# Performance work log

Measured on AMD Instinct MI355X. Metric: run time of the kernel, lower is better.

The kernel has to match this reference:

```python
import jax, jax.numpy as jnp
import numpy as np

N = 100000
E = 1600000
IN_DIM = 128
H = 64
OUT_DIM = 64
EPS = 1e-5


def batch_norm(x, gamma, beta):
    # BatchNorm1d with batch statistics (training-mode normalization, biased var)
    mu = jnp.mean(x, axis=0)
    var = jnp.var(x, axis=0)
    return (x - mu) * jax.lax.rsqrt(var + EPS) * gamma + beta


def gcn_conv(x, src, dst, W, b, n_nodes):
    # PyG GCNConv: add self-loops, symmetric deg^-1/2 normalization, X W, scatter-add, bias
    loop = jnp.arange(n_nodes, dtype=src.dtype)
    s = jnp.concatenate([src, loop])
    d = jnp.concatenate([dst, loop])
    w = jnp.ones(s.shape[0], dtype=x.dtype)
    deg = jax.ops.segment_sum(w, d, num_segments=n_nodes)
    dinv = jnp.where(deg > 0, jax.lax.rsqrt(deg), 0.0)
    norm = dinv[s] * w * dinv[d]                      # [E+N]
    h = x @ W                                         # [N, out]
    msg = h[s] * norm[:, None]                        # [E+N, out]
    out = jax.ops.segment_sum(msg, d, num_segments=n_nodes)
    return out + b


def setup_inputs() -> dict:
    key = jax.random.key(0)
    ks = jax.random.split(key, 12)
    x = jax.random.normal(ks[0], (N, IN_DIM), dtype=jnp.float32)
    edge_index = jax.random.randint(ks[1], (2, E), 0, N, dtype=jnp.int64)
    s = 0.05
    return {
        "x": x,
        "edge_index": edge_index,
        "bn_in_g": jnp.ones((IN_DIM,), jnp.float32),
        "bn_in_b": jnp.zeros((IN_DIM,), jnp.float32),
        "Wp": jax.random.normal(ks[2], (IN_DIM, H), jnp.float32) * s,
        "bp": jnp.zeros((H,), jnp.float32),
        "W1": jax.random.normal(ks[3], (H, H), jnp.float32) * s,
        "b1": jnp.zeros((H,), jnp.float32),
        "bn1_g": jnp.ones((H,), jnp.float32),
        "bn1_b": jnp.zeros((H,), jnp.float32),
        "W2": jax.random.normal(ks[4], (H, OUT_DIM), jnp.float32) * s,
        "b2": jnp.zeros((OUT_DIM,), jnp.float32),
        "bn2_g": jnp.ones((OUT_DIM,), jnp.float32),
        "bn2_b": jnp.zeros((OUT_DIM,), jnp.float32),
    }


def reference(x, edge_index, bn_in_g, bn_in_b, Wp, bp, W1, b1, bn1_g, bn1_b, W2, b2, bn2_g, bn2_b):
    src, dst = edge_index[0], edge_index[1]
    n = x.shape[0]
    h0 = batch_norm(x, bn_in_g, bn_in_b)
    h0 = jax.nn.relu(h0 @ Wp + bp)
    h1 = gcn_conv(h0, src, dst, W1, b1, n)
    h1 = jax.nn.relu(batch_norm(h1, bn1_g, bn1_b))
    # dropout in eval mode: identity
    h2 = gcn_conv(h1, src, dst, W2, b2, n)
    return batch_norm(h2, bn2_g, bn2_b)
```

## Files before the change

kernel.cpp:

```cpp
#include <hip/hip_runtime.h>
#include <hip/hip_bf16.h>

#define EPS 1e-5f
#define CAP 6144
#define PCHUNK 4096
#define XP 68

__device__ __forceinline__ void acc_q(float* acc, uint2 v, float s) {
    acc[0] += s * (float)((int)(v.x << 24) >> 24);
    acc[1] += s * (float)((int)(v.x << 16) >> 24);
    acc[2] += s * (float)((int)(v.x << 8) >> 24);
    acc[3] += s * (float)((int)v.x >> 24);
    acc[4] += s * (float)((int)(v.y << 24) >> 24);
    acc[5] += s * (float)((int)(v.y << 16) >> 24);
    acc[6] += s * (float)((int)(v.y << 8) >> 24);
    acc[7] += s * (float)((int)v.y >> 24);
}

#define GEMM_KK(kk, wvec)                                                        \
    {                                                                            \
        float a0 = (kk == 0) ? xv0.x : (kk == 1) ? xv0.y : (kk == 2) ? xv0.z : xv0.w; \
        float a1 = (kk == 0) ? xv1.x : (kk == 1) ? xv1.y : (kk == 2) ? xv1.z : xv1.w; \
        float a2 = (kk == 0) ? xv2.x : (kk == 1) ? xv2.y : (kk == 2) ? xv2.z : xv2.w; \
        float a3 = (kk == 0) ? xv3.x : (kk == 1) ? xv3.y : (kk == 2) ? xv3.z : xv3.w; \
        acc[0][0] += a0 * wvec.x; acc[0][1] += a0 * wvec.y;                      \
        acc[0][2] += a0 * wvec.z; acc[0][3] += a0 * wvec.w;                      \
        acc[1][0] += a1 * wvec.x; acc[1][1] += a1 * wvec.y;                      \
        acc[1][2] += a1 * wvec.z; acc[1][3] += a1 * wvec.w;                      \
        acc[2][0] += a2 * wvec.x; acc[2][1] += a2 * wvec.y;                      \
        acc[2][2] += a2 * wvec.z; acc[2][3] += a2 * wvec.w;                      \
        acc[3][0] += a3 * wvec.x; acc[3][1] += a3 * wvec.y;                      \
        acc[3][2] += a3 * wvec.z; acc[3][3] += a3 * wvec.w;                      \
    }

__global__ void k_init(int* __restrict__ cur, float* __restrict__ stats) {
    int t = threadIdx.x;
    stats[t] = 0.0f;
    cur[t] = t * CAP;
}

__global__ __launch_bounds__(256) void k_A(
    const int* __restrict__ src, const int* __restrict__ dst,
    int* __restrict__ cur, unsigned* __restrict__ packbuf, int E, int NBP,
    const float* __restrict__ x, float* __restrict__ xsum, float* __restrict__ xsq, int N) {
    __shared__ int h[512], delta[512], wsc[4];
    __shared__ unsigned buf[PCHUNK];
    __shared__ int addr[PCHUNK];
    int tx = threadIdx.x;
    if ((int)blockIdx.x < NBP) {
        int e0 = blockIdx.x * PCHUNK;
        int e1 = min(e0 + PCHUNK, E);
        int csize = e1 - e0;
        h[tx] = 0; h[tx + 256] = 0;
        __syncthreads();
        for (int e = e0 + tx; e < e1; e += 256)
            atomicAdd(&h[dst[e] >> 8], 1);
        __syncthreads();
        int b0 = tx * 2;
        int c0 = h[b0], c1 = h[b0 + 1];
        int tsum = c0 + c1;
        int lane = tx & 63, wid = tx >> 6;
        int v = tsum;
#pragma unroll
        for (int off = 1; off < 64; off <<= 1) {
            int u = __shfl_up(v, off);
            if (lane >= off) v += u;
        }
        if (lane == 63) wsc[wid] = v;
        __syncthreads();
        int wbase = 0;
        for (int w = 0; w < wid; w++) wbase += wsc[w];
        int excl0 = wbase + v - tsum;
        int excl1 = excl0 + c0;
        if (c0 > 0) delta[b0] = atomicAdd(&cur[b0], c0) - excl0;
        if (c1 > 0) delta[b0 + 1] = atomicAdd(&cur[b0 + 1], c1) - excl1;
        __syncthreads();
        h[b0] = excl0; h[b0 + 1] = excl1;
        __syncthreads();
        for (int e = e0 + tx; e < e1; e += 256) {
            int d = dst[e];
            int b = d >> 8;
            int rank = atomicAdd(&h[b], 1);
            buf[rank] = ((unsigned)src[e] << 8) | (unsigned)(d & 255);
            addr[rank] = delta[b];
        }
        __syncthreads();
        for (int i = tx; i < csize; i += 256)
            packbuf[addr[i] + i] = buf[i];
    } else {
        float* ls = (float*)buf;
        float* lq = ls + 256;
        int b2 = blockIdx.x - NBP;
        int col = tx & 127, half = tx >> 7;
        float s = 0.f, q = 0.f;
        for (int r = b2 * 2 + half; r < N; r += 1024) {
            float v = x[(long long)r * 128 + col];
            s += v; q += v * v;
        }
        ls[tx] = s; lq[tx] = q;
        __syncthreads();
        if (half == 0) {
            s = ls[tx] + ls[tx + 128];
            q = lq[tx] + lq[tx + 128];
            atomicAdd(&xsum[col], s);
            atomicAdd(&xsq[col], q);
        }
    }
}

__global__ __launch_bounds__(512) void k_B(
    const unsigned* __restrict__ packbuf, const int* __restrict__ cur,
    int2* __restrict__ rowbe, int* __restrict__ rowmid, float* __restrict__ dinv,
    int* __restrict__ eidx, int NB, int N, int Nh,
    const float* __restrict__ x, const float* __restrict__ stats,
    const float* __restrict__ g, const float* __restrict__ bbn,
    const float* __restrict__ Wp, const float* __restrict__ bp,
    float* __restrict__ H, float invN) {
    __shared__ __align__(16) char smem[52224];
    int tx = threadIdx.x;
    if ((int)blockIdx.x < NB) {
        int* cnt  = (int*)smem;
        int* loff = cnt + 512;
        int* wsum = loff + 512;
        int b = blockIdx.x;
        int base = b * CAP;
        int end = cur[b];
        cnt[tx] = 0;
        __syncthreads();
        for (int e = base + tx; e < end; e += 512) {
            unsigned pk = packbuf[e];
            int key = (((int)pk & 255) << 1) | (int)((pk >> 8) >= (unsigned)Nh);
            atomicAdd(&cnt[key], 1);
        }
        __syncthreads();
        int c = cnt[tx];
        int lane = tx & 63, wid = tx >> 6;
        int v = c;
#pragma unroll
        for (int off = 1; off < 64; off <<= 1) {
            int u = __shfl_up(v, off);
            if (lane >= off) v += u;
        }
        if (lane == 63) wsum[wid] = v;
        __syncthreads();
        int wbase = 0;
        for (int w = 0; w < wid; w++) wbase += wsum[w];
        int excl = wbase + v - c;
        loff[tx] = excl;
        __syncthreads();
        if (tx < 256) {
            int node = b * 256 + tx;
            if (node < N) {
                int beg = base + loff[2 * tx];
                int mid = base + loff[2 * tx + 1];
                int e2 = mid + cnt[2 * tx + 1];
                rowbe[node] = make_int2(beg, e2);
                rowmid[node] = mid;
                int deg = cnt[2 * tx] + cnt[2 * tx + 1];
                dinv[node] = rsqrtf(1.0f + (float)deg);
            }
        }
        __syncthreads();
        for (int e = base + tx; e < end; e += 512) {
            unsigned pk = packbuf[e];
            int key = (((int)pk & 255) << 1) | (int)((pk >> 8) >= (unsigned)Nh);
            int pos = atomicAdd(&loff[key], 1);
            eidx[base + pos] = (int)(pk >> 8);
        }
    } else {
        float* xs  = (float*)smem;
        float* ws  = xs + 128 * XP;
        float* scb = ws + 4096;
        float* shb = scb + 128;
        if (tx < 128) {
            float mu = stats[tx] * invN;
            float var = stats[128 + tx] * invN - mu * mu;
            float s = g[tx] * rsqrtf(var + EPS);
            scb[tx] = s;
            shb[tx] = bbn[tx] - mu * s;
        }
        __syncthreads();
        int r0 = ((int)blockIdx.x - NB) * 128;
        int cw = tx & 15, rw = tx >> 4;
        float acc[4][4];
#pragma unroll
        for (int j = 0; j < 4; j++)
#pragma unroll
            for (int i = 0; i < 4; i++) acc[j][i] = 0.f;

#pragma unroll 1
        for (int kc = 0; kc < 128; kc += 64) {
#pragma unroll
            for (int i = 0; i < 4; i++) {
                int f = tx + 512 * i;
                int row = f >> 4, kq = f & 15;
                int rr = r0 + row;
                float4 v = make_float4(0.f, 0.f, 0.f, 0.f);
                if (rr < N) v = ((const float4*)(x + (long long)rr * 128 + kc))[kq];
                int cb = kc + kq * 4;
                v.x = v.x * scb[cb + 0] + shb[cb + 0];
                v.y = v.y * scb[cb + 1] + shb[cb + 1];
                v.z = v.z * scb[cb + 2] + shb[cb + 2];
                v.w = v.w * scb[cb + 3] + shb[cb + 3];
                *(float4*)&xs[row * XP + kq * 4] = v;
            }
#pragma unroll
            for (int i = 0; i < 2; i++) {
                int f = tx + 512 * i;
                int k = f >> 4, cq = f & 15;
                float4 w = ((const float4*)(Wp + (long long)(kc + k) * 64))[cq];
                *(float4*)&ws[k * 64 + cq * 4] = w;
            }
            __syncthreads();
#pragma unroll 1
            for (int k4 = 0; k4 < 16; k4++) {
                float4 xv0 = *(const float4*)&xs[(rw * 4 + 0) * XP + k4 * 4];
                float4 xv1 = *(const float4*)&xs[(rw * 4 + 1) * XP + k4 * 4];
                float4 xv2 = *(const float4*)&xs[(rw * 4 + 2) * XP + k4 * 4];
                float4 xv3 = *(const float4*)&xs[(rw * 4 + 3) * XP + k4 * 4];
#pragma unroll
                for (int kk = 0; kk < 4; kk++) {
                    float4 w = *(const float4*)&ws[(k4 * 4 + kk) * 64 + cw * 4];
                    GEMM_KK(kk, w);
                }
            }
            __syncthreads();
        }
        float4 bpv = ((const float4*)bp)[cw];
#pragma unroll
        for (int j = 0; j < 4; j++) {
            int rr = r0 + rw * 4 + j;
            if (rr < N) {
                float4 o;
                o.x = fmaxf(acc[j][0] + bpv.x, 0.f);
                o.y = fmaxf(acc[j][1] + bpv.y, 0.f);
                o.z = fmaxf(acc[j][2] + bpv.z, 0.f);
                o.w = fmaxf(acc[j][3] + bpv.w, 0.f);
                ((float4*)(H + (long long)rr * 64))[cw] = o;
            }
        }
    }
}

template <bool BNRELU>
__global__ __launch_bounds__(512) void k_gemm_scale(
    const float* __restrict__ In, const float* __restrict__ W,
    const float* __restrict__ dinv, const float* __restrict__ ssum,
    const float* __restrict__ ssq, const float* __restrict__ g,
    const float* __restrict__ bb, float invN, unsigned* __restrict__ Bq,
    float* __restrict__ S, int N) {
    __shared__ __align__(16) char smem[52224];
    float* xs  = (float*)smem;
    float* ws  = xs + 128 * XP;
    float* scb = ws + 4096;
    float* shb = scb + 128;
    int tx = threadIdx.x;
    if (BNRELU) {
        if (tx < 64) {
            float mu = ssum[tx] * invN;
            float var = ssq[tx] * invN - mu * mu;
            float s = g[tx] * rsqrtf(var + EPS);
            scb[tx] = s;
            shb[tx] = bb[tx] - mu * s;
        }
        __syncthreads();
    }
    int r0 = blockIdx.x * 128;
    int cw = tx & 15, rw = tx >> 4;
#pragma unroll
    for (int i = 0; i < 4; i++) {
        int f = tx + 512 * i;
        int row = f >> 4, kq = f & 15;
        int rr = r0 + row;
        float4 v = make_float4(0.f, 0.f, 0.f, 0.f);
        if (rr < N) v = ((const float4*)(In + (long long)rr * 64))[kq];
        if (BNRELU) {
            int cb = kq * 4;
            v.x = fmaxf(v.x * scb[cb + 0] + shb[cb + 0], 0.f);
            v.y = fmaxf(v.y * scb[cb + 1] + shb[cb + 1], 0.f);
            v.z = fmaxf(v.z * scb[cb + 2] + shb[cb + 2], 0.f);
            v.w = fmaxf(v.w * scb[cb + 3] + shb[cb + 3], 0.f);
        }
        *(float4*)&xs[row * XP + kq * 4] = v;
    }
#pragma unroll
    for (int i = 0; i < 2; i++) {
        int f = tx + 512 * i;
        int k = f >> 4, cq = f & 15;
        float4 w = ((const float4*)(W + (long long)k * 64))[cq];
        *(float4*)&ws[k * 64 + cq * 4] = w;
    }
    __syncthreads();
    float acc[4][4];
#pragma unroll
    for (int j = 0; j < 4; j++)
#pragma unroll
        for (int i = 0; i < 4; i++) acc[j][i] = 0.f;
#pragma unroll 1
    for (int k4 = 0; k4 < 16; k4++) {
        float4 xv0 = *(const float4*)&xs[(rw * 4 + 0) * XP + k4 * 4];
        float4 xv1 = *(const float4*)&xs[(rw * 4 + 1) * XP + k4 * 4];
        float4 xv2 = *(const float4*)&xs[(rw * 4 + 2) * XP + k4 * 4];
        float4 xv3 = *(const float4*)&xs[(rw * 4 + 3) * XP + k4 * 4];
#pragma unroll
        for (int kk = 0; kk < 4; kk++) {
            float4 w = *(const float4*)&ws[(k4 * 4 + kk) * 64 + cw * 4];
            GEMM_KK(kk, w);
        }
    }
#pragma unroll
    for (int j = 0; j < 4; j++) {
        int rr = r0 + rw * 4 + j;
        float dv = (rr < N) ? dinv[rr] : 0.f;
        float m = 0.f;
#pragma unroll
        for (int i = 0; i < 4; i++) {
            acc[j][i] *= dv;
            m = fmaxf(m, fabsf(acc[j][i]));
        }
#pragma unroll
        for (int mask = 1; mask < 16; mask <<= 1)
            m = fmaxf(m, __shfl_xor(m, mask, 64));
        float inv = (m > 0.f) ? (127.0f / m) : 0.f;
        if (rr < N) {
            if (cw == 0) S[rr] = m * (1.0f / 127.0f);
            int q0 = (int)rintf(acc[j][0] * inv);
            int q1 = (int)rintf(acc[j][1] * inv);
            int q2 = (int)rintf(acc[j][2] * inv);
            int q3 = (int)rintf(acc[j][3] * inv);
            unsigned w = ((unsigned)q0 & 255u) | (((unsigned)q1 & 255u) << 8) |
                         (((unsigned)q2 & 255u) << 16) | (((unsigned)q3 & 255u) << 24);
            Bq[(long long)rr * 16 + cw] = w;
        }
    }
}

__global__ __launch_bounds__(256) void k_gather_finish(
    const uint2* __restrict__ Q, const float* __restrict__ S,
    const int2* __restrict__ rowbe, const int* __restrict__ rowmid,
    const int* __restrict__ eidx,
    const float* __restrict__ dinv, const float* __restrict__ bias,
    float* __restrict__ Out, float* __restrict__ ssum, float* __restrict__ ssq,
    int N, int Nh) {
    int tx = threadIdx.x;
    int g = tx >> 3;
    int l = tx & 7;
    int d = blockIdx.x * 32 + g;

    float s[8], q[8];
#pragma unroll
    for (int j = 0; j < 8; j++) { s[j] = 0.f; q[j] = 0.f; }

    if (d < N) {
        int2 be = rowbe[d];
        int mid = rowmid[d];
        uint2 v0 = Q[(long long)d * 8 + l];
        float sd = S[d];
        float dv = dinv[d];

        float acc[8];
#pragma unroll
        for (int j = 0; j < 8; j++) acc[j] = 0.f;

        for (int seg = 0; seg < 2; seg++) {
            int k  = seg ? mid : be.x;
            int ke = seg ? be.y : mid;
            if (k >= ke) continue;
            int dmy = seg ? Nh : 0;
            int idx_cur[8];
#pragma unroll
            for (int j = 0; j < 8; j++)
                idx_cur[j] = (k + j < ke) ? eidx[k + j] : dmy;

            while (k < ke) {
                uint2 bb[8];
                float sv[8];
#pragma unroll
                for (int j = 0; j < 8; j++)
                    bb[j] = Q[(long long)idx_cur[j] * 8 + l];
#pragma unroll
                for (int j = 0; j < 8; j++)
                    sv[j] = (k + j < ke) ? S[idx_cur[j]] : 0.f;
                int kn = k + 8;
                int idx_nxt[8];
#pragma unroll
                for (int j = 0; j < 8; j++)
                    idx_nxt[j] = (kn + j < ke) ? eidx[kn + j] : dmy;
#pragma unroll
                for (int j = 0; j < 8; j++)
                    acc_q(acc, bb[j], sv[j]);
#pragma unroll
                for (int j = 0; j < 8; j++) idx_cur[j] = idx_nxt[j];
                k = kn;
            }
        }
        acc_q(acc, v0, sd);

        float4 o0, o1;
#pragma unroll
        for (int j = 0; j < 8; j++) {
            float v = acc[j] * dv + bias[8 * l + j];
            ((j < 4) ? (&o0.x)[j] : (&o1.x)[j - 4]) = v;
            s[j] += v; q[j] += v * v;
        }
        float4* outp = (float4*)(Out + (long long)d * 64 + 8 * l);
        outp[0] = o0;
        outp[1] = o1;
    }

#pragma unroll
    for (int m = 8; m <= 32; m <<= 1) {
#pragma unroll
        for (int j = 0; j < 8; j++) {
            s[j] += __shfl_xor(s[j], m, 64);
            q[j] += __shfl_xor(q[j], m, 64);
        }
    }
    __shared__ float ws_s[4][64], ws_q[4][64];
    int wv = tx >> 6, ln = tx & 63;
    if (ln < 8) {
#pragma unroll
        for (int j = 0; j < 8; j++) {
            ws_s[wv][ln * 8 + j] = s[j];
            ws_q[wv][ln * 8 + j] = q[j];
        }
    }
    __syncthreads();
    if (tx < 64) {
        float S2 = ws_s[0][tx] + ws_s[1][tx] + ws_s[2][tx] + ws_s[3][tx];
        float Q2 = ws_q[0][tx] + ws_q[1][tx] + ws_q[2][tx] + ws_q[3][tx];
        atomicAdd(&ssum[tx], S2);
        atomicAdd(&ssq[tx], Q2);
    }
}

__global__ __launch_bounds__(256) void k_final(const float* __restrict__ In,
                                               const float* __restrict__ ssum,
                                               const float* __restrict__ ssq,
                                               const float* __restrict__ g,
                                               const float* __restrict__ bb, float invN,
                                               float* __restrict__ out, int total4) {
    __shared__ float scs[64], shs[64];
    int tx = threadIdx.x;
    if (tx < 64) {
        float mu = ssum[tx] * invN;
        float var = ssq[tx] * invN - mu * mu;
        float s = g[tx] * rsqrtf(var + EPS);
        scs[tx] = s;
        shs[tx] = bb[tx] - mu * s;
    }
    __syncthreads();
    int t = blockIdx.x * blockDim.x + tx;
    if (t < total4) {
        float4 v = ((const float4*)In)[t];
        int j = (t * 4) & 63;
        v.x = v.x * scs[j + 0] + shs[j + 0];
        v.y = v.y * scs[j + 1] + shs[j + 1];
        v.z = v.z * scs[j + 2] + shs[j + 2];
        v.w = v.w * scs[j + 3] + shs[j + 3];
        ((float4*)out)[t] = v;
    }
}

extern "C" void kernel_launch(void* const* d_in, const int* in_sizes, int n_in,
                              void* d_out, int out_size, void* d_ws, size_t ws_size,
                              hipStream_t stream) {
    const float* x       = (const float*)d_in[0];
    const int*   ei      = (const int*)d_in[1];
    const float* bn_in_g = (const float*)d_in[2];
    const float* bn_in_b = (const float*)d_in[3];
    const float* Wp      = (const float*)d_in[4];
    const float* bp      = (const float*)d_in[5];
    const float* W1      = (const float*)d_in[6];
    const float* b1      = (const float*)d_in[7];
    const float* bn1_g   = (const float*)d_in[8];
    const float* bn1_b   = (const float*)d_in[9];
    const float* W2      = (const float*)d_in[10];
    const float* b2      = (const float*)d_in[11];
    const float* bn2_g   = (const float*)d_in[12];
    const float* bn2_b   = (const float*)d_in[13];

    int N = in_sizes[0] / 128;
    int E = in_sizes[1] / 2;
    const int* src = ei;
    const int* dst = ei + E;
    int Nh  = N >> 1;
    int NB  = (N + 255) >> 8;
    int NBP = (E + PCHUNK - 1) / PCHUNK;
    int ntg = (N + 127) / 128;

    long long Npad = ((long long)N + 128) & ~127LL;
    int*   cur    = (int*)d_ws;
    float* stats  = (float*)(cur + 512);
    int2*  rowbe  = (int2*)(stats + 512);
    float* dinv   = (float*)(rowbe + Npad);
    int*   rowmid = (int*)(dinv + Npad);
    float* S      = (float*)(rowmid + Npad);
    unsigned* packbuf = (unsigned*)(S + Npad);
    int*   eidx   = (int*)(packbuf + (long long)NB * CAP);
    unsigned* Bq  = (unsigned*)(eidx + (long long)NB * CAP);
    float* H      = (float*)d_out;

    int gb = (N + 31) / 32;
    float invN = 1.0f / (float)N;

    k_init<<<1, 512, 0, stream>>>(cur, stats);
    k_A<<<NBP + 512, 256, 0, stream>>>(src, dst, cur, packbuf, E, NBP,
                                       x, stats, stats + 128, N);
    k_B<<<NB + ntg, 512, 0, stream>>>(packbuf, cur, rowbe, rowmid, dinv, eidx, NB, N, Nh,
                                      x, stats, bn_in_g, bn_in_b, Wp, bp, H, invN);

    k_gemm_scale<false><<<ntg, 512, 0, stream>>>(H, W1, dinv, nullptr, nullptr, nullptr,
                                                 nullptr, invN, Bq, S, N);
    k_gather_finish<<<gb, 256, 0, stream>>>((const uint2*)Bq, S, rowbe, rowmid, eidx, dinv,
                                            b1, H, stats + 256, stats + 320, N, Nh);

    k_gemm_scale<true><<<ntg, 512, 0, stream>>>(H, W2, dinv, stats + 256, stats + 320,
                                                bn1_g, bn1_b, invN, Bq, S, N);
    k_gather_finish<<<gb, 256, 0, stream>>>((const uint2*)Bq, S, rowbe, rowmid, eidx, dinv,
                                            b2, H, stats + 384, stats + 448, N, Nh);

    k_final<<<(N * 16 + 255) / 256, 256, 0, stream>>>(H, stats + 384, stats + 448,
                                                      bn2_g, bn2_b, invN, H, N * 16);
}
```

Measured before the change: 432.5 us.

## Split GCN gather into two passes over source-index halves for cache locality

The single gather kernel, which walked both edge segments (sources below and above Nh) per destination row, is split into two launches. The first pass gathers only the low-half sources and writes partial sums to H. The second pass reloads those partials, gathers the high-half sources, then applies dinv, bias and the batch-norm statistics. The aim is to keep each pass's gather working set (half of the quantized feature table) resident in cache, at the cost of an extra launch and an extra read and write of H.

```diff
diff --git a/kernel.cpp b/kernel.cpp
--- a/kernel.cpp
+++ b/kernel.cpp
@@ -335,12 +335,13 @@
     }
 }
 
-__global__ __launch_bounds__(256) void k_gather_finish(
+template <int PASS>
+__global__ __launch_bounds__(256) void k_gather_pass(
     const uint2* __restrict__ Q, const float* __restrict__ S,
     const int2* __restrict__ rowbe, const int* __restrict__ rowmid,
     const int* __restrict__ eidx,
     const float* __restrict__ dinv, const float* __restrict__ bias,
-    float* __restrict__ Out, float* __restrict__ ssum, float* __restrict__ ssq,
+    float* __restrict__ H, float* __restrict__ ssum, float* __restrict__ ssq,
     int N, int Nh) {
     int tx = threadIdx.x;
     int g = tx >> 3;
@@ -348,30 +349,37 @@
     int d = blockIdx.x * 32 + g;
 
     float s[8], q[8];
-#pragma unroll
-    for (int j = 0; j < 8; j++) { s[j] = 0.f; q[j] = 0.f; }
+    if (PASS == 1) {
+#pragma unroll
+        for (int j = 0; j < 8; j++) { s[j] = 0.f; q[j] = 0.f; }
+    }
 
     if (d < N) {
         int2 be = rowbe[d];
         int mid = rowmid[d];
-        uint2 v0 = Q[(long long)d * 8 + l];
-        float sd = S[d];
-        float dv = dinv[d];
-
         float acc[8];
-#pragma unroll
-        for (int j = 0; j < 8; j++) acc[j] = 0.f;
-
-        for (int seg = 0; seg < 2; seg++) {
-            int k  = seg ? mid : be.x;
-            int ke = seg ? be.y : mid;
-            if (k >= ke) continue;
-            int dmy = seg ? Nh : 0;
+        float4* hp = (float4*)(H + (long long)d * 64 + 8 * l);
+
+        int k, ke, dmy;
+        if (PASS == 0) {
+            uint2 v0 = Q[(long long)d * 8 + l];
+            float sd = S[d];
+#pragma unroll
+            for (int j = 0; j < 8; j++) acc[j] = 0.f;
+            acc_q(acc, v0, sd);
+            k = be.x; ke = mid; dmy = 0;
+        } else {
+            float4 p0 = hp[0], p1 = hp[1];
+            acc[0] = p0.x; acc[1] = p0.y; acc[2] = p0.z; acc[3] = p0.w;
+            acc[4] = p1.x; acc[5] = p1.y; acc[6] = p1.z; acc[7] = p1.w;
+            k = mid; ke = be.y; dmy = Nh;
+        }
+
+        if (k < ke) {
             int idx_cur[8];
 #pragma unroll
             for (int j = 0; j < 8; j++)
                 idx_cur[j] = (k + j < ke) ? eidx[k + j] : dmy;
-
             while (k < ke) {
                 uint2 bb[8];
                 float sv[8];
@@ -394,43 +402,52 @@
                 k = kn;
             }
         }
-        acc_q(acc, v0, sd);
-
-        float4 o0, o1;
-#pragma unroll
-        for (int j = 0; j < 8; j++) {
-            float v = acc[j] * dv + bias[8 * l + j];
-            ((j < 4) ? (&o0.x)[j] : (&o1.x)[j - 4]) = v;
-            s[j] += v; q[j] += v * v;
-        }
-        float4* outp = (float4*)(Out + (long long)d * 64 + 8 * l);
-        outp[0] = o0;
-        outp[1] = o1;
-    }
-
-#pragma unroll
-    for (int m = 8; m <= 32; m <<= 1) {
-#pragma unroll
-        for (int j = 0; j < 8; j++) {
-            s[j] += __shfl_xor(s[j], m, 64);
-            q[j] += __shfl_xor(q[j], m, 64);
-        }
-    }
-    __shared__ float ws_s[4][64], ws_q[4][64];
-    int wv = tx >> 6, ln = tx & 63;
-    if (ln < 8) {
-#pragma unroll
-        for (int j = 0; j < 8; j++) {
-            ws_s[wv][ln * 8 + j] = s[j];
-            ws_q[wv][ln * 8 + j] = q[j];
-        }
-    }
-    __syncthreads();
-    if (tx < 64) {
-        float S2 = ws_s[0][tx] + ws_s[1][tx] + ws_s[2][tx] + ws_s[3][tx];
-        float Q2 = ws_q[0][tx] + ws_q[1][tx] + ws_q[2][tx] + ws_q[3][tx];
-        atomicAdd(&ssum[tx], S2);
-        atomicAdd(&ssq[tx], Q2);
+
+        if (PASS == 0) {
+            float4 o0, o1;
+            o0.x = acc[0]; o0.y = acc[1]; o0.z = acc[2]; o0.w = acc[3];
+            o1.x = acc[4]; o1.y = acc[5]; o1.z = acc[6]; o1.w = acc[7];
+            hp[0] = o0;
+            hp[1] = o1;
+        } else {
+            float dv = dinv[d];
+            float4 o0, o1;
+#pragma unroll
+            for (int j = 0; j < 8; j++) {
+                float v = acc[j] * dv + bias[8 * l + j];
+                ((j < 4) ? (&o0.x)[j] : (&o1.x)[j - 4]) = v;
+                s[j] += v; q[j] += v * v;
+            }
+            hp[0] = o0;
+            hp[1] = o1;
+        }
+    }
+
+    if (PASS == 1) {
+#pragma unroll
+        for (int m = 8; m <= 32; m <<= 1) {
+#pragma unroll
+            for (int j = 0; j < 8; j++) {
+                s[j] += __shfl_xor(s[j], m, 64);
+                q[j] += __shfl_xor(q[j], m, 64);
+            }
+        }
+        __shared__ float ws_s[4][64], ws_q[4][64];
+        int wv = tx >> 6, ln = tx & 63;
+        if (ln < 8) {
+#pragma unroll
+            for (int j = 0; j < 8; j++) {
+                ws_s[wv][ln * 8 + j] = s[j];
+                ws_q[wv][ln * 8 + j] = q[j];
+            }
+        }
+        __syncthreads();
+        if (tx < 64) {
+            float S2 = ws_s[0][tx] + ws_s[1][tx] + ws_s[2][tx] + ws_s[3][tx];
+            float Q2 = ws_q[0][tx] + ws_q[1][tx] + ws_q[2][tx] + ws_q[3][tx];
+            atomicAdd(&ssum[tx], S2);
+            atomicAdd(&ssq[tx], Q2);
+        }
     }
 }
 
@@ -512,13 +529,17 @@
 
     k_gemm_scale<false><<<ntg, 512, 0, stream>>>(H, W1, dinv, nullptr, nullptr, nullptr,
                                                  nullptr, invN, Bq, S, N);
-    k_gather_finish<<<gb, 256, 0, stream>>>((const uint2*)Bq, S, rowbe, rowmid, eidx, dinv,
-                                            b1, H, stats + 256, stats + 320, N, Nh);
+    k_gather_pass<0><<<gb, 256, 0, stream>>>((const uint2*)Bq, S, rowbe, rowmid, eidx,
+                                             dinv, b1, H, stats + 256, stats + 320, N, Nh);
+    k_gather_pass<1><<<gb, 256, 0, stream>>>((const uint2*)Bq, S, rowbe, rowmid, eidx,
+                                             dinv, b1, H, stats + 256, stats + 320, N, Nh);
 
     k_gemm_scale<true><<<ntg, 512, 0, stream>>>(H, W2, dinv, stats + 256, stats + 320,
                                                 bn1_g, bn1_b, invN, Bq, S, N);
-    k_gather_finish<<<gb, 256, 0, stream>>>((const uint2*)Bq, S, rowbe, rowmid, eidx, dinv,
-                                            b2, H, stats + 384, stats + 448, N, Nh);
+    k_gather_pass<0><<<gb, 256, 0, stream>>>((const uint2*)Bq, S, rowbe, rowmid, eidx,
+                                             dinv, b2, H, stats + 384, stats + 448, N, Nh);
+    k_gather_pass<1><<<gb, 256, 0, stream>>>((const uint2*)Bq, S, rowbe, rowmid, eidx,
+                                             dinv, b2, H, stats + 384, stats + 448, N, Nh);
 
     k_final<<<(N * 16 + 255) / 256, 256, 0, stream>>>(H, stats + 384, stats + 448,
                                                       bn2_g, bn2_b, invN, H, N * 16);
```

Measured after the change: 468.6 us. 1.08x slower.

## Fuse first GCN weight GEMM and int8 quantization into projection kernel

Applied to the files above, without the earlier changes.

The projection GEMM blocks in k_B now keep the ReLU output tile in shared memory, multiply it by W1 directly, and write per-row int8-quantized rows plus row scales. This removes the separate k_gemm_scale pass and the round trip of the 100k x 64 float intermediate through global memory. The dinv scaling, which in k_B is not yet available to GEMM blocks because it is computed concurrently by the CSR blocks, moves to a new small k_scale kernel. The cost is more shared-memory work and longer GEMM blocks inside the mixed k_B launch.

```diff
diff --git a/kernel.cpp b/kernel.cpp
--- a/kernel.cpp
+++ b/kernel.cpp
@@ -115,7 +115,8 @@
     const float* __restrict__ x, const float* __restrict__ stats,
     const float* __restrict__ g, const float* __restrict__ bbn,
     const float* __restrict__ Wp, const float* __restrict__ bp,
-    float* __restrict__ H, float invN) {
+    const float* __restrict__ W1, unsigned* __restrict__ Bq, float* __restrict__ S,
+    float invN) {
     __shared__ __align__(16) char smem[52224];
     int tx = threadIdx.x;
     if ((int)blockIdx.x < NB) {
@@ -229,17 +230,65 @@
         float4 bpv = ((const float4*)bp)[cw];
 #pragma unroll
         for (int j = 0; j < 4; j++) {
+            float4 o;
+            o.x = fmaxf(acc[j][0] + bpv.x, 0.f);
+            o.y = fmaxf(acc[j][1] + bpv.y, 0.f);
+            o.z = fmaxf(acc[j][2] + bpv.z, 0.f);
+            o.w = fmaxf(acc[j][3] + bpv.w, 0.f);
+            *(float4*)&xs[(rw * 4 + j) * XP + cw * 4] = o;
+        }
+#pragma unroll
+        for (int i = 0; i < 2; i++) {
+            int f = tx + 512 * i;
+            int k = f >> 4, cq = f & 15;
+            float4 w = ((const float4*)(W1 + (long long)k * 64))[cq];
+            *(float4*)&ws[k * 64 + cq * 4] = w;
+        }
+        __syncthreads();
+#pragma unroll
+        for (int j = 0; j < 4; j++)
+#pragma unroll
+            for (int i = 0; i < 4; i++) acc[j][i] = 0.f;
+#pragma unroll 1
+        for (int k4 = 0; k4 < 16; k4++) {
+            float4 xv0 = *(const float4*)&xs[(rw * 4 + 0) * XP + k4 * 4];
+            float4 xv1 = *(const float4*)&xs[(rw * 4 + 1) * XP + k4 * 4];
+            float4 xv2 = *(const float4*)&xs[(rw * 4 + 2) * XP + k4 * 4];
+            float4 xv3 = *(const float4*)&xs[(rw * 4 + 3) * XP + k4 * 4];
+#pragma unroll
+            for (int kk = 0; kk < 4; kk++) {
+                float4 w = *(const float4*)&ws[(k4 * 4 + kk) * 64 + cw * 4];
+                GEMM_KK(kk, w);
+            }
+        }
+#pragma unroll
+        for (int j = 0; j < 4; j++) {
             int rr = r0 + rw * 4 + j;
+            float m = 0.f;
+#pragma unroll
+            for (int i = 0; i < 4; i++) m = fmaxf(m, fabsf(acc[j][i]));
+#pragma unroll
+            for (int mask = 1; mask < 16; mask <<= 1)
+                m = fmaxf(m, __shfl_xor(m, mask, 64));
+            float inv = (m > 0.f) ? (127.0f / m) : 0.f;
             if (rr < N) {
-                float4 o;
-                o.x = fmaxf(acc[j][0] + bpv.x, 0.f);
-                o.y = fmaxf(acc[j][1] + bpv.y, 0.f);
-                o.z = fmaxf(acc[j][2] + bpv.z, 0.f);
-                o.w = fmaxf(acc[j][3] + bpv.w, 0.f);
-                ((float4*)(H + (long long)rr * 64))[cw] = o;
-            }
-        }
-    }
+                if (cw == 0) S[rr] = m * (1.0f / 127.0f);
+                int q0 = (int)rintf(acc[j][0] * inv);
+                int q1 = (int)rintf(acc[j][1] * inv);
+                int q2 = (int)rintf(acc[j][2] * inv);
+                int q3 = (int)rintf(acc[j][3] * inv);
+                unsigned w = ((unsigned)q0 & 255u) | (((unsigned)q1 & 255u) << 8) |
+                             (((unsigned)q2 & 255u) << 16) | (((unsigned)q3 & 255u) << 24);
+                Bq[(long long)rr * 16 + cw] = w;
+            }
+        }
+    }
+}
+
+__global__ __launch_bounds__(256) void k_scale(float* __restrict__ S,
+                                               const float* __restrict__ dinv, int N) {
+    int r = blockIdx.x * 256 + threadIdx.x;
+    if (r < N) S[r] *= dinv[r];
 }
 
 template <bool BNRELU>
@@ -508,10 +557,8 @@
     k_A<<<NBP + 512, 256, 0, stream>>>(src, dst, cur, packbuf, E, NBP,
                                        x, stats, stats + 128, N);
     k_B<<<NB + ntg, 512, 0, stream>>>(packbuf, cur, rowbe, rowmid, dinv, eidx, NB, N, Nh,
-                                      x, stats, bn_in_g, bn_in_b, Wp, bp, H, invN);
-
-    k_gemm_scale<false><<<ntg, 512, 0, stream>>>(H, W1, dinv, nullptr, nullptr, nullptr,
-                                                 nullptr, invN, Bq, S, N);
+                                      x, stats, bn_in_g, bn_in_b, Wp, bp, W1, Bq, S, invN);
+    k_scale<<<(N + 255) / 256, 256, 0, stream>>>(S, dinv, N);
     k_gather_finish<<<gb, 256, 0, stream>>>((const uint2*)Bq, S, rowbe, rowmid, eidx, dinv,
                                             b1, H, stats + 256, stats + 320, N, Nh);
 
```

Measured after the change: 430.2 us. No clear change (-0.5%).
